# Kernel tuning notes

Hardware: AMD Instinct MI355X
Metric: run time of the kernel (lower is better)

## Reference

```python
import jax, jax.numpy as jnp
import numpy as np

BATCH = 262144
N_ASSETS = 64
N_GROUPS = 8
ITERS = 20
EPS = 1e-9


def setup_inputs() -> dict:
    key = jax.random.key(0)
    kx = jax.random.fold_in(key, 1)
    x = jax.random.uniform(kx, (BATCH, N_ASSETS), dtype=jnp.float32)
    x = x / jnp.sum(x, axis=-1, keepdims=True)  # roughly simplex-like raw weights
    box_lb = jnp.zeros((N_ASSETS,), jnp.float32)          # port_type[0] = 0 (long-only)
    box_ub = jnp.full((N_ASSETS,), 0.3, jnp.float32)      # per-asset cap from _build_constraints
    # one-hot group membership matrix: asset i belongs to group i % N_GROUPS
    gid = np.arange(N_ASSETS) % N_GROUPS
    A = np.zeros((N_GROUPS, N_ASSETS), np.float32)
    A[gid, np.arange(N_ASSETS)] = 1.0
    group_A = jnp.asarray(A)
    group_lb = jnp.full((N_GROUPS,), 0.05, jnp.float32)
    group_ub = jnp.full((N_GROUPS,), 0.5, jnp.float32)
    return {"x": x, "box_lb": box_lb, "box_ub": box_ub, "group_A": group_A,
            "group_lb": group_lb, "group_ub": group_ub, "num_iterations": ITERS}


def _dykstra(x, box_lb, box_ub, group_A, group_lb, group_ub, num_iterations):
    n = x.shape[-1]
    norm_sq = jnp.sum(group_A * group_A, axis=-1)  # (G,)

    def box_simplex(w):
        w = jnp.clip(w, box_lb, box_ub)
        return w - (jnp.sum(w, axis=-1, keepdims=True) - 1.0) / n

    def group_step(w, g):
        a, lb, ub, ns = g  # a: (N,), scalars lb/ub/ns
        Aw = w @ a  # (B,)
        w = jnp.where((Aw > ub)[:, None], w - ((Aw - ub) / (ns + EPS))[:, None] * a, w)
        Aw = w @ a  # recomputed on updated w, matching the TF layer
        w = jnp.where((Aw < lb)[:, None], w - ((Aw - lb) / (ns + EPS))[:, None] * a, w)
        return w, None

    def body(i, w):
        w = box_simplex(w)
        w, _ = jax.lax.scan(group_step, w, (group_A, group_lb, group_ub, norm_sq))
        return w

    w = jax.lax.fori_loop(0, num_iterations, body, x)
    return box_simplex(w)


def reference(x, box_lb, box_ub, group_A, group_lb, group_ub, num_iterations):
    return _dykstra(x, box_lb, box_ub, group_A, group_lb, group_ub, num_iterations)
```

## Files before the change

### kernel.cpp

```cpp
#include <hip/hip_runtime.h>


#define NA 64
#define NG 8
#define TOL 1e-6f
#define RS 72
#define ROWS_PER_BLOCK 32
#define ROWS_PER_WAVE 8

__device__ __forceinline__ float row8_allreduce_sum(float v) {
    int j = __builtin_amdgcn_update_dpp(0, __builtin_bit_cast(int, v),
                                        0xB1 , 0xF, 0xF, true);
    v += __builtin_bit_cast(float, j);
    j = __builtin_amdgcn_update_dpp(0, __builtin_bit_cast(int, v),
                                    0x4E , 0xF, 0xF, true);
    v += __builtin_bit_cast(float, j);
    j = __builtin_amdgcn_ds_swizzle(__builtin_bit_cast(int, v), 0x101F );
    v += __builtin_bit_cast(float, j);
    return v;
}

__global__ __launch_bounds__(256) void proj_kernel(
    const float* __restrict__ x,
    const float* __restrict__ box_lb,
    const float* __restrict__ box_ub,
    const float* __restrict__ group_A,
    const float* __restrict__ group_lb,
    const float* __restrict__ group_ub,
    const int*  __restrict__ num_iter,
    float* __restrict__ out,
    int nrows)
{
    __shared__ float lds[ROWS_PER_BLOCK * RS];

    const int tid  = threadIdx.x;
    const int wave = tid >> 6;
    const int lane = tid & 63;
    const int lr   = lane >> 3;
    const int c    = lane & 7;

    const size_t wrow0 = (size_t)blockIdx.x * ROWS_PER_BLOCK + (size_t)wave * ROWS_PER_WAVE;
    const size_t r = wrow0 + (size_t)lr;
    const bool fullwave = (wrow0 + ROWS_PER_WAVE) <= (size_t)nrows;
    const bool valid = r < (size_t)nrows;

    float* lw = lds + wave * ROWS_PER_WAVE * RS;

    float4 v0, v1;
    if (fullwave) {
        const float4* src = reinterpret_cast<const float4*>(x + wrow0 * NA);
        v0 = src[lane];
        v1 = src[lane + 64];
    }

    const float lb0 = box_lb[0], ub0 = box_ub[0];
    bool ok = (box_lb[lane] == lb0) && (box_ub[lane] == ub0) && (lb0 <= ub0);
#pragma unroll
    for (int g = 0; g < NG; ++g) {
        const float expect = ((lane & 7) == g) ? 1.0f : 0.0f;
        ok = ok && (group_A[g * NA + lane] == expect);
    }
    const bool fast = __all(ok);

    if (fullwave) {
        *reinterpret_cast<float4*>(lw + (lane >> 4) * RS + (lane & 15) * 4) = v0;
        *reinterpret_cast<float4*>(lw + ((lane >> 4) + 4) * RS + (lane & 15) * 4) = v1;
    }
    __syncthreads();
    float w[8];
    if (fullwave) {
#pragma unroll
        for (int k = 0; k < 8; ++k) w[k] = lw[lr * RS + k * 8 + c];
    } else if (valid) {
#pragma unroll
        for (int k = 0; k < 8; ++k) w[k] = x[r * NA + k * 8 + c];
    }

    const int iters = *num_iter;
    float shift = 0.0f;

    if (fast) {
        const float glb = group_lb[c];
        const float gub = group_ub[c];
        const float inv8 = 1.0f / (8.0f + 1e-9f);

        for (int it = 0; it < iters; ++it) {
#pragma unroll
            for (int k = 0; k < 8; ++k)
                w[k] = __builtin_amdgcn_fmed3f(w[k], lb0, ub0);
            const float s01 = w[0] + w[1], s23 = w[2] + w[3];
            const float s45 = w[4] + w[5], s67 = w[6] + w[7];
            const float dota = (s01 + s23) + (s45 + s67);

            const float S = row8_allreduce_sum(dota);
            const float sh = fmaf(S, 1.0f / NA, -1.0f / NA);

            const float Aw  = fmaf(-8.0f, sh, dota);
            const float e1  = fmaxf(Aw - gub, 0.0f);
            const float Aw2 = Aw - e1;
            const float e2  = fminf(Aw2 - glb, 0.0f);
            const float d   = (e1 + e2) * inv8;
            const float u   = sh + d;
#pragma unroll
            for (int k = 0; k < 8; ++k) w[k] -= u;

            if (__all(__builtin_fabsf(sh) < TOL && __builtin_fabsf(d) < TOL))
                break;
        }
#pragma unroll
        for (int k = 0; k < 8; ++k)
            w[k] = __builtin_amdgcn_fmed3f(w[k], lb0, ub0);
        const float s01 = w[0] + w[1], s23 = w[2] + w[3];
        const float s45 = w[4] + w[5], s67 = w[6] + w[7];
        const float S = row8_allreduce_sum((s01 + s23) + (s45 + s67));
        shift = fmaf(S, 1.0f / NA, -1.0f / NA);
    } else {
        float lbv[8], ubv[8];
#pragma unroll
        for (int k = 0; k < 8; ++k) {
            lbv[k] = box_lb[k * 8 + c];
            ubv[k] = box_ub[k * 8 + c];
        }
        for (int it = 0; it < iters; ++it) {
            float S = 0.0f;
#pragma unroll
            for (int k = 0; k < 8; ++k) {
                w[k] = fminf(fmaxf(w[k], lbv[k]), ubv[k]);
                S += w[k];
            }
            S = row8_allreduce_sum(S);
            const float sh = (S - 1.0f) * (1.0f / NA);
#pragma unroll
            for (int k = 0; k < 8; ++k) w[k] -= sh;

            for (int g = 0; g < NG; ++g) {
                float a[8];
#pragma unroll
                for (int k = 0; k < 8; ++k) a[k] = group_A[g * NA + k * 8 + c];
                float ns = 0.0f, Aw = 0.0f;
#pragma unroll
                for (int k = 0; k < 8; ++k) {
                    ns = fmaf(a[k], a[k], ns);
                    Aw = fmaf(a[k], w[k], Aw);
                }
                ns = row8_allreduce_sum(ns);
                Aw = row8_allreduce_sum(Aw);
                const float invg = 1.0f / (ns + 1e-9f);
                const float gub = group_ub[g], glb = group_lb[g];
                const float d1 = (Aw > gub) ? (Aw - gub) * invg : 0.0f;
#pragma unroll
                for (int k = 0; k < 8; ++k) w[k] = fmaf(-d1, a[k], w[k]);
                float Aw2 = 0.0f;
#pragma unroll
                for (int k = 0; k < 8; ++k) Aw2 = fmaf(a[k], w[k], Aw2);
                Aw2 = row8_allreduce_sum(Aw2);
                const float d2 = (Aw2 < glb) ? (Aw2 - glb) * invg : 0.0f;
#pragma unroll
                for (int k = 0; k < 8; ++k) w[k] = fmaf(-d2, a[k], w[k]);
            }
        }
        float S = 0.0f;
#pragma unroll
        for (int k = 0; k < 8; ++k) {
            w[k] = fminf(fmaxf(w[k], lbv[k]), ubv[k]);
            S += w[k];
        }
        S = row8_allreduce_sum(S);
        shift = (S - 1.0f) * (1.0f / NA);
    }

    if (fullwave) {
#pragma unroll
        for (int k = 0; k < 8; ++k)
            lw[lr * RS + k * 8 + c] = w[k] - shift;
    }
    __syncthreads();
    if (fullwave) {
        const float4 q0 = *reinterpret_cast<const float4*>(lw + (lane >> 4) * RS + (lane & 15) * 4);
        const float4 q1 = *reinterpret_cast<const float4*>(lw + ((lane >> 4) + 4) * RS + (lane & 15) * 4);
        float4* dst = reinterpret_cast<float4*>(out + wrow0 * NA);
        dst[lane] = q0;
        dst[lane + 64] = q1;
    } else if (valid) {
#pragma unroll
        for (int k = 0; k < 8; ++k)
            out[r * NA + k * 8 + c] = w[k] - shift;
    }
}

extern "C" void kernel_launch(void* const* d_in, const int* in_sizes, int n_in,
                              void* d_out, int out_size, void* d_ws, size_t ws_size,
                              hipStream_t stream) {
    const float* x        = (const float*)d_in[0];
    const float* box_lb   = (const float*)d_in[1];
    const float* box_ub   = (const float*)d_in[2];
    const float* group_A  = (const float*)d_in[3];
    const float* group_lb = (const float*)d_in[4];
    const float* group_ub = (const float*)d_in[5];
    const int*   num_iter = (const int*)d_in[6];
    float* out = (float*)d_out;

    const int nrows = in_sizes[0] / NA;
    const int total = nrows * 8;
    const int block = 256;
    const int grid = (total + block - 1) / block;

    proj_kernel<<<grid, block, 0, stream>>>(x, box_lb, box_ub, group_A,
                                            group_lb, group_ub, num_iter,
                                            out, nrows);
}
```

Baseline: 127.9 us.

## Drop LDS transpose; load contiguous row chunks and reduce groups across lanes

Each lane now loads 8 contiguous floats of its row directly with float4 loads and stores them back the same way. This removes the LDS staging buffer and both block barriers. Because each lane's 8 values now belong to 8 different groups, the fast path has to run 8 per-group butterfly reductions (24 DPP adds) every iteration instead of one row-sum reduction. The final reduction step switches from ds_swizzle to a DPP half-row mirror, and group bounds are preloaded into registers. The trade is less memory-staging overhead against more cross-lane ALU work and register pressure inside the iteration loop.

Measured after the change: 128.9 us. Within noise of the previous version (+0.8%).

```diff
diff --git a/kernel.cpp b/kernel.cpp
--- a/kernel.cpp
+++ b/kernel.cpp
@@ -4,19 +4,18 @@
 #define NA 64
 #define NG 8
 #define TOL 1e-6f
-#define RS 72
-#define ROWS_PER_BLOCK 32
-#define ROWS_PER_WAVE 8
-
-__device__ __forceinline__ float row8_allreduce_sum(float v) {
-    int j = __builtin_amdgcn_update_dpp(0, __builtin_bit_cast(int, v),
-                                        0xB1 , 0xF, 0xF, true);
-    v += __builtin_bit_cast(float, j);
-    j = __builtin_amdgcn_update_dpp(0, __builtin_bit_cast(int, v),
-                                    0x4E , 0xF, 0xF, true);
-    v += __builtin_bit_cast(float, j);
-    j = __builtin_amdgcn_ds_swizzle(__builtin_bit_cast(int, v), 0x101F );
-    v += __builtin_bit_cast(float, j);
+
+template <int CTRL>
+__device__ __forceinline__ float dpp_add(float v) {
+    const int o = __builtin_amdgcn_update_dpp(0, __builtin_bit_cast(int, v),
+                                              CTRL, 0xF, 0xF, true);
+    return v + __builtin_bit_cast(float, o);
+}
+
+__device__ __forceinline__ float row8_allreduce(float v) {
+    v = dpp_add<0xB1>(v);
+    v = dpp_add<0x4E>(v);
+    v = dpp_add<0x141>(v);
     return v;
 }
 
@@ -31,26 +30,21 @@
     float* __restrict__ out,
     int nrows)
 {
-    __shared__ float lds[ROWS_PER_BLOCK * RS];
-
-    const int tid  = threadIdx.x;
-    const int wave = tid >> 6;
-    const int lane = tid & 63;
-    const int lr   = lane >> 3;
-    const int c    = lane & 7;
-
-    const size_t wrow0 = (size_t)blockIdx.x * ROWS_PER_BLOCK + (size_t)wave * ROWS_PER_WAVE;
-    const size_t r = wrow0 + (size_t)lr;
-    const bool fullwave = (wrow0 + ROWS_PER_WAVE) <= (size_t)nrows;
-    const bool valid = r < (size_t)nrows;
-
-    float* lw = lds + wave * ROWS_PER_WAVE * RS;
-
-    float4 v0, v1;
-    if (fullwave) {
-        const float4* src = reinterpret_cast<const float4*>(x + wrow0 * NA);
-        v0 = src[lane];
-        v1 = src[lane + 64];
+    const int t = blockIdx.x * blockDim.x + threadIdx.x;
+    const int r = t >> 3;
+    const int c = t & 7;
+    const int lane = threadIdx.x & 63;
+    if (r >= nrows) return;
+
+    const float* __restrict__ xr = x + (size_t)r * NA + c * 8;
+    float* __restrict__ outr = out + (size_t)r * NA + c * 8;
+
+    float w[8];
+    {
+        const float4 v0 = *reinterpret_cast<const float4*>(xr);
+        const float4 v1 = *reinterpret_cast<const float4*>(xr + 4);
+        w[0] = v0.x; w[1] = v0.y; w[2] = v0.z; w[3] = v0.w;
+        w[4] = v1.x; w[5] = v1.y; w[6] = v1.z; w[7] = v1.w;
     }
 
     const float lb0 = box_lb[0], ub0 = box_ub[0];
@@ -62,49 +56,50 @@
     }
     const bool fast = __all(ok);
 
-    if (fullwave) {
-        *reinterpret_cast<float4*>(lw + (lane >> 4) * RS + (lane & 15) * 4) = v0;
-        *reinterpret_cast<float4*>(lw + ((lane >> 4) + 4) * RS + (lane & 15) * 4) = v1;
-    }
-    __syncthreads();
-    float w[8];
-    if (fullwave) {
-#pragma unroll
-        for (int k = 0; k < 8; ++k) w[k] = lw[lr * RS + k * 8 + c];
-    } else if (valid) {
-#pragma unroll
-        for (int k = 0; k < 8; ++k) w[k] = x[r * NA + k * 8 + c];
-    }
+    float glb_s[NG], gub_s[NG];
+#pragma unroll
+    for (int g = 0; g < NG; ++g) { glb_s[g] = group_lb[g]; gub_s[g] = group_ub[g]; }
 
     const int iters = *num_iter;
     float shift = 0.0f;
 
     if (fast) {
-        const float glb = group_lb[c];
-        const float gub = group_ub[c];
         const float inv8 = 1.0f / (8.0f + 1e-9f);
 
         for (int it = 0; it < iters; ++it) {
 #pragma unroll
             for (int k = 0; k < 8; ++k)
                 w[k] = __builtin_amdgcn_fmed3f(w[k], lb0, ub0);
-            const float s01 = w[0] + w[1], s23 = w[2] + w[3];
-            const float s45 = w[4] + w[5], s67 = w[6] + w[7];
-            const float dota = (s01 + s23) + (s45 + s67);
-
-            const float S = row8_allreduce_sum(dota);
+
+            float gs[NG];
+#pragma unroll
+            for (int k = 0; k < 8; ++k) gs[k] = w[k];
+#pragma unroll
+            for (int k = 0; k < 8; ++k) gs[k] = dpp_add<0xB1>(gs[k]);
+#pragma unroll
+            for (int k = 0; k < 8; ++k) gs[k] = dpp_add<0x4E>(gs[k]);
+#pragma unroll
+            for (int k = 0; k < 8; ++k) gs[k] = dpp_add<0x141>(gs[k]);
+
+            const float S = ((gs[0] + gs[1]) + (gs[2] + gs[3]))
+                          + ((gs[4] + gs[5]) + (gs[6] + gs[7]));
             const float sh = fmaf(S, 1.0f / NA, -1.0f / NA);
 
-            const float Aw  = fmaf(-8.0f, sh, dota);
-            const float e1  = fmaxf(Aw - gub, 0.0f);
-            const float Aw2 = Aw - e1;
-            const float e2  = fminf(Aw2 - glb, 0.0f);
-            const float d   = (e1 + e2) * inv8;
-            const float u   = sh + d;
-#pragma unroll
-            for (int k = 0; k < 8; ++k) w[k] -= u;
-
-            if (__all(__builtin_fabsf(sh) < TOL && __builtin_fabsf(d) < TOL))
+            float u[NG], dmax = 0.0f;
+#pragma unroll
+            for (int g = 0; g < NG; ++g) {
+                const float Aw  = fmaf(-8.0f, sh, gs[g]);
+                const float e1  = fmaxf(Aw - gub_s[g], 0.0f);
+                const float Aw2 = Aw - e1;
+                const float e2  = fminf(Aw2 - glb_s[g], 0.0f);
+                const float d   = (e1 + e2) * inv8;
+                u[g] = sh + d;
+                dmax = fmaxf(dmax, __builtin_fabsf(d));
+            }
+#pragma unroll
+            for (int k = 0; k < 8; ++k) w[k] -= u[k];
+
+            if (__all(__builtin_fabsf(sh) < TOL && dmax < TOL))
                 break;
         }
 #pragma unroll
@@ -112,14 +107,19 @@
             w[k] = __builtin_amdgcn_fmed3f(w[k], lb0, ub0);
         const float s01 = w[0] + w[1], s23 = w[2] + w[3];
         const float s45 = w[4] + w[5], s67 = w[6] + w[7];
-        const float S = row8_allreduce_sum((s01 + s23) + (s45 + s67));
+        const float S = row8_allreduce((s01 + s23) + (s45 + s67));
         shift = fmaf(S, 1.0f / NA, -1.0f / NA);
     } else {
         float lbv[8], ubv[8];
-#pragma unroll
-        for (int k = 0; k < 8; ++k) {
-            lbv[k] = box_lb[k * 8 + c];
-            ubv[k] = box_ub[k * 8 + c];
+        {
+            const float4 a0 = *reinterpret_cast<const float4*>(box_lb + c * 8);
+            const float4 a1 = *reinterpret_cast<const float4*>(box_lb + c * 8 + 4);
+            const float4 b0 = *reinterpret_cast<const float4*>(box_ub + c * 8);
+            const float4 b1 = *reinterpret_cast<const float4*>(box_ub + c * 8 + 4);
+            lbv[0]=a0.x; lbv[1]=a0.y; lbv[2]=a0.z; lbv[3]=a0.w;
+            lbv[4]=a1.x; lbv[5]=a1.y; lbv[6]=a1.z; lbv[7]=a1.w;
+            ubv[0]=b0.x; ubv[1]=b0.y; ubv[2]=b0.z; ubv[3]=b0.w;
+            ubv[4]=b1.x; ubv[5]=b1.y; ubv[6]=b1.z; ubv[7]=b1.w;
         }
         for (int it = 0; it < iters; ++it) {
             float S = 0.0f;
@@ -128,32 +128,36 @@
                 w[k] = fminf(fmaxf(w[k], lbv[k]), ubv[k]);
                 S += w[k];
             }
-            S = row8_allreduce_sum(S);
+            S = row8_allreduce(S);
             const float sh = (S - 1.0f) * (1.0f / NA);
 #pragma unroll
             for (int k = 0; k < 8; ++k) w[k] -= sh;
 
             for (int g = 0; g < NG; ++g) {
                 float a[8];
-#pragma unroll
-                for (int k = 0; k < 8; ++k) a[k] = group_A[g * NA + k * 8 + c];
+                {
+                    const float4 q0 = *reinterpret_cast<const float4*>(group_A + g * NA + c * 8);
+                    const float4 q1 = *reinterpret_cast<const float4*>(group_A + g * NA + c * 8 + 4);
+                    a[0]=q0.x; a[1]=q0.y; a[2]=q0.z; a[3]=q0.w;
+                    a[4]=q1.x; a[5]=q1.y; a[6]=q1.z; a[7]=q1.w;
+                }
                 float ns = 0.0f, Aw = 0.0f;
 #pragma unroll
                 for (int k = 0; k < 8; ++k) {
                     ns = fmaf(a[k], a[k], ns);
                     Aw = fmaf(a[k], w[k], Aw);
                 }
-                ns = row8_allreduce_sum(ns);
-                Aw = row8_allreduce_sum(Aw);
+                ns = row8_allreduce(ns);
+                Aw = row8_allreduce(Aw);
                 const float invg = 1.0f / (ns + 1e-9f);
-                const float gub = group_ub[g], glb = group_lb[g];
+                const float gub = gub_s[g], glb = glb_s[g];
                 const float d1 = (Aw > gub) ? (Aw - gub) * invg : 0.0f;
 #pragma unroll
                 for (int k = 0; k < 8; ++k) w[k] = fmaf(-d1, a[k], w[k]);
                 float Aw2 = 0.0f;
 #pragma unroll
                 for (int k = 0; k < 8; ++k) Aw2 = fmaf(a[k], w[k], Aw2);
-                Aw2 = row8_allreduce_sum(Aw2);
+                Aw2 = row8_allreduce(Aw2);
                 const float d2 = (Aw2 < glb) ? (Aw2 - glb) * invg : 0.0f;
 #pragma unroll
                 for (int k = 0; k < 8; ++k) w[k] = fmaf(-d2, a[k], w[k]);
@@ -165,26 +169,18 @@
             w[k] = fminf(fmaxf(w[k], lbv[k]), ubv[k]);
             S += w[k];
         }
-        S = row8_allreduce_sum(S);
+        S = row8_allreduce(S);
         shift = (S - 1.0f) * (1.0f / NA);
     }
 
-    if (fullwave) {
-#pragma unroll
-        for (int k = 0; k < 8; ++k)
-            lw[lr * RS + k * 8 + c] = w[k] - shift;
-    }
-    __syncthreads();
-    if (fullwave) {
-        const float4 q0 = *reinterpret_cast<const float4*>(lw + (lane >> 4) * RS + (lane & 15) * 4);
-        const float4 q1 = *reinterpret_cast<const float4*>(lw + ((lane >> 4) + 4) * RS + (lane & 15) * 4);
-        float4* dst = reinterpret_cast<float4*>(out + wrow0 * NA);
-        dst[lane] = q0;
-        dst[lane + 64] = q1;
-    } else if (valid) {
-#pragma unroll
-        for (int k = 0; k < 8; ++k)
-            out[r * NA + k * 8 + c] = w[k] - shift;
+    {
+        float4 v0, v1;
+        v0.x = w[0] - shift; v0.y = w[1] - shift;
+        v0.z = w[2] - shift; v0.w = w[3] - shift;
+        v1.x = w[4] - shift; v1.y = w[5] - shift;
+        v1.z = w[6] - shift; v1.w = w[7] - shift;
+        *reinterpret_cast<float4*>(outr) = v0;
+        *reinterpret_cast<float4*>(outr + 4) = v1;
     }
 }
 
```
